# Kernel optimization log

Measured on AMD Instinct MI355X. Metric: run time of the kernel, lower is better.

Reference implementation:

```python
import jax, jax.numpy as jnp
import numpy as np

GROUP_SIZE = 128
ZERO_POINT = 8  # 4-bit symmetric zero point


def setup_inputs() -> dict:
    key = jax.random.key(0)
    k1, k2, k3, k4, k5, k6 = jax.random.split(key, 6)
    B, S, IN, OUT, RANK = 4, 2048, 4096, 4096, 32
    n_groups = IN // GROUP_SIZE  # 32
    x = jax.random.normal(k1, (B, S, IN), dtype=jnp.float32)
    q = jax.random.randint(k2, (OUT, IN), 0, 16, dtype=jnp.int32)  # 4-bit codes
    scales = jax.random.uniform(k3, (OUT, n_groups), dtype=jnp.float32)
    U = jax.random.normal(k4, (OUT, RANK), dtype=jnp.float32)
    V = jax.random.normal(k5, (RANK, IN), dtype=jnp.float32)
    bias = jax.random.normal(k6, (OUT,), dtype=jnp.float32)
    return {"x": x, "q": q, "scales": scales, "U": U, "V": V, "bias": bias}


def reference(x, q, scales, U, V, bias):
    out_f, in_f = q.shape
    n_groups = scales.shape[1]
    # Dequantize: per-group scaled 4-bit codes -> [out, in]
    qf = (q.astype(scales.dtype) - ZERO_POINT).reshape(out_f, n_groups, GROUP_SIZE)
    W = (qf * scales[:, :, None]).reshape(out_f, in_f)
    # Low-rank correction
    W = W + U @ V
    # F.linear: y = x @ W^T + b
    return jnp.einsum("bsi,oi->bso", x, W) + bias
```

## Files before the change

### kernel.cpp

```cpp
#include <hip/hip_runtime.h>
#include <hip/hip_bf16.h>

#define GAS __attribute__((address_space(1)))
#define LAS __attribute__((address_space(3)))

typedef __bf16 bf16x8 __attribute__((ext_vector_type(8)));
typedef float f32x4 __attribute__((ext_vector_type(4)));

constexpr int Kd = 4096;
constexpr int Nd = 4096;
constexpr int RANKd = 32;
constexpr int NGroups = 32;
constexpr int BM = 128, BN = 128, BK = 32;

constexpr int BWR = 32;
constexpr int BWC = 256;

__global__ __launch_bounds__(256) void build_w(
    const int* __restrict__ q, const float* __restrict__ scales,
    const float* __restrict__ U, const float* __restrict__ V,
    __hip_bfloat16* __restrict__ W)
{
  __shared__ float V_s[RANKd][BWC + 4];
  __shared__ float U_s[BWR][RANKd + 1];

  const int t  = threadIdx.x;
  const int n0 = blockIdx.y * BWR;
  const int k0 = blockIdx.x * BWC;

  {
    const int idx = t * 4;
    const int row = idx >> 5, rr = idx & 31;
    float4 uv = *(const float4*)(U + (size_t)(n0 + row) * RANKd + rr);
    U_s[row][rr] = uv.x; U_s[row][rr + 1] = uv.y;
    U_s[row][rr + 2] = uv.z; U_s[row][rr + 3] = uv.w;
  }
  #pragma unroll
  for (int i = 0; i < 8; ++i) {
    const int idx = i * 1024 + t * 4;
    const int vr = idx >> 8, vc = idx & 255;
    float4 vv = *(const float4*)(V + (size_t)vr * Kd + k0 + vc);
    *(float4*)&V_s[vr][vc] = vv;
  }
  __syncthreads();

  const int rs   = t >> 5;
  const int cs   = t & 31;
  const int row0 = n0 + rs * 4;
  const int kc   = k0 + cs * 8;
  const int grp  = kc >> 7;

  float acc[4][8];
  #pragma unroll
  for (int j = 0; j < 4; ++j) {
    const int4* q4 = (const int4*)(q + (size_t)(row0 + j) * Kd + kc);
    int4 a = q4[0], b = q4[1];
    const float sc = scales[(size_t)(row0 + j) * NGroups + grp];
    acc[j][0] = (float)(a.x - 8) * sc; acc[j][1] = (float)(a.y - 8) * sc;
    acc[j][2] = (float)(a.z - 8) * sc; acc[j][3] = (float)(a.w - 8) * sc;
    acc[j][4] = (float)(b.x - 8) * sc; acc[j][5] = (float)(b.y - 8) * sc;
    acc[j][6] = (float)(b.z - 8) * sc; acc[j][7] = (float)(b.w - 8) * sc;
  }

  #pragma unroll 4
  for (int r = 0; r < RANKd; ++r) {
    float4 v0 = *(const float4*)&V_s[r][cs * 8];
    float4 v1 = *(const float4*)&V_s[r][cs * 8 + 4];
    #pragma unroll
    for (int j = 0; j < 4; ++j) {
      const float u = U_s[rs * 4 + j][r];
      acc[j][0] += u * v0.x; acc[j][1] += u * v0.y;
      acc[j][2] += u * v0.z; acc[j][3] += u * v0.w;
      acc[j][4] += u * v1.x; acc[j][5] += u * v1.y;
      acc[j][6] += u * v1.z; acc[j][7] += u * v1.w;
    }
  }

  #pragma unroll
  for (int j = 0; j < 4; ++j) {
    union { __hip_bfloat16 h[8]; int4 v; } o;
    #pragma unroll
    for (int i = 0; i < 8; ++i) o.h[i] = __float2bfloat16(acc[j][i]);
    *(int4*)(W + (size_t)(row0 + j) * Kd + kc) = o.v;
  }
}

__global__ __launch_bounds__(256) void convert_x(
    const float* __restrict__ x, __hip_bfloat16* __restrict__ xb)
{
  const size_t i = ((size_t)blockIdx.x * 256 + threadIdx.x) * 8;
  float4 a = *(const float4*)(x + i);
  float4 b = *(const float4*)(x + i + 4);
  union { __hip_bfloat16 h[8]; int4 v; } u;
  u.h[0] = __float2bfloat16(a.x); u.h[1] = __float2bfloat16(a.y);
  u.h[2] = __float2bfloat16(a.z); u.h[3] = __float2bfloat16(a.w);
  u.h[4] = __float2bfloat16(b.x); u.h[5] = __float2bfloat16(b.y);
  u.h[6] = __float2bfloat16(b.z); u.h[7] = __float2bfloat16(b.w);
  *(int4*)(xb + i) = u.v;
}

template <bool ABF16>
__global__ __launch_bounds__(256) void gemm_bt(
    const void* __restrict__ Ap, const __hip_bfloat16* __restrict__ Bt,
    const float* __restrict__ bias, float* __restrict__ C)
{
  __shared__ __hip_bfloat16 As[BM * BK];
  __shared__ __hip_bfloat16 Bs[BN * BK];

  const int t  = threadIdx.x;
  const int l  = t & 63;
  const int w  = t >> 6;
  const int wm = w >> 1;
  const int wn = w & 1;
  const int bm0 = blockIdx.y * BM;
  const int bn0 = blockIdx.x * BN;

  f32x4 acc[4][4];
  #pragma unroll
  for (int i = 0; i < 4; ++i)
    #pragma unroll
    for (int j = 0; j < 4; ++j)
      acc[i][j] = (f32x4){0.f, 0.f, 0.f, 0.f};

  const __hip_bfloat16* Abf = (const __hip_bfloat16*)Ap;
  const float*          A32 = (const float*)Ap;

  const int srow  = w * 16 + (l >> 2);
  const int schnk = (l & 3) ^ ((l >> 3) & 3);
  const __hip_bfloat16* ag0 = Abf + (size_t)(bm0 + srow) * Kd + schnk * 8;
  const __hip_bfloat16* bg0 = Bt  + (size_t)(bn0 + srow) * Kd + schnk * 8;
  char* asb = (char*)As + w * 1024;
  char* bsb = (char*)Bs + w * 1024;

  const int arow = t >> 1;
  const int apair = (t & 1);
  const float* a32p = A32 + (size_t)(bm0 + arow) * Kd + apair * 16;
  const int aswz = (arow >> 1) & 3;
  __hip_bfloat16* asw0 = As + arow * BK + (((apair * 2 + 0) ^ aswz) * 8);
  __hip_bfloat16* asw1 = As + arow * BK + (((apair * 2 + 1) ^ aswz) * 8);

  const int rlow = l & 15;
  const int rd_a = (wm * 64 + rlow) * 64 + (((l >> 4) ^ ((l >> 1) & 3)) * 16);
  const int rd_b = (wn * 64 + rlow) * 64 + (((l >> 4) ^ ((l >> 1) & 3)) * 16);

  for (int kt = 0; kt < Kd / BK; ++kt) {
    if constexpr (ABF16) {
      const __hip_bfloat16* ag = ag0 + kt * BK;
      __builtin_amdgcn_global_load_lds((GAS void*)ag,           (LAS void*)asb,          16, 0, 0);
      __builtin_amdgcn_global_load_lds((GAS void*)(ag + 64*Kd), (LAS void*)(asb + 4096), 16, 0, 0);
    } else {
      const float* ap = a32p + kt * BK;
      float4 f0 = ((const float4*)ap)[0];
      float4 f1 = ((const float4*)ap)[1];
      union { __hip_bfloat16 h[8]; int4 v; } u0, u1;
      u0.h[0]=__float2bfloat16(f0.x); u0.h[1]=__float2bfloat16(f0.y);
      u0.h[2]=__float2bfloat16(f0.z); u0.h[3]=__float2bfloat16(f0.w);
      u1.h[0]=__float2bfloat16(f1.x); u1.h[1]=__float2bfloat16(f1.y);
      u1.h[2]=__float2bfloat16(f1.z); u1.h[3]=__float2bfloat16(f1.w);
      *(int4*)asw0 = u0.v;
      *(int4*)asw1 = u1.v;
    }
    {
      const __hip_bfloat16* bg = bg0 + kt * BK;
      __builtin_amdgcn_global_load_lds((GAS void*)bg,           (LAS void*)bsb,          16, 0, 0);
      __builtin_amdgcn_global_load_lds((GAS void*)(bg + 64*Kd), (LAS void*)(bsb + 4096), 16, 0, 0);
    }

    __syncthreads();

    bf16x8 af[4], bf[4];
    #pragma unroll
    for (int i = 0; i < 4; ++i)
      af[i] = *(const bf16x8*)((const char*)As + rd_a + i * 1024);
    #pragma unroll
    for (int j = 0; j < 4; ++j)
      bf[j] = *(const bf16x8*)((const char*)Bs + rd_b + j * 1024);

    #pragma unroll
    for (int i = 0; i < 4; ++i)
      #pragma unroll
      for (int j = 0; j < 4; ++j)
        acc[i][j] = __builtin_amdgcn_mfma_f32_16x16x32_bf16(af[i], bf[j], acc[i][j], 0, 0, 0);

    __syncthreads();
  }

  const int colbase = bn0 + wn * 64 + (l & 15);
  const int rowbase = bm0 + wm * 64 + (l >> 4) * 4;
  #pragma unroll
  for (int j = 0; j < 4; ++j) {
    const int col = colbase + j * 16;
    const float bz = bias[col];
    #pragma unroll
    for (int i = 0; i < 4; ++i) {
      const int row0 = rowbase + i * 16;
      #pragma unroll
      for (int r = 0; r < 4; ++r)
        C[(size_t)(row0 + r) * Nd + col] = acc[i][j][r] + bz;
    }
  }
}

extern "C" void kernel_launch(void* const* d_in, const int* in_sizes, int n_in,
                              void* d_out, int out_size, void* d_ws, size_t ws_size,
                              hipStream_t stream)
{
  const float* x      = (const float*)d_in[0];
  const int*   q      = (const int*)  d_in[1];
  const float* scales = (const float*)d_in[2];
  const float* U      = (const float*)d_in[3];
  const float* V      = (const float*)d_in[4];
  const float* bias   = (const float*)d_in[5];
  float* out = (float*)d_out;

  const int M = in_sizes[0] / Kd;

  __hip_bfloat16* Wb = (__hip_bfloat16*)d_ws;
  const size_t wbytes = (size_t)Nd * Kd * sizeof(__hip_bfloat16);
  const size_t xbytes = (size_t)M  * Kd * sizeof(__hip_bfloat16);

  build_w<<<dim3(Kd / BWC, Nd / BWR), dim3(256), 0, stream>>>(q, scales, U, V, Wb);

  dim3 grid(Nd / BN, M / BM);
  if (ws_size >= wbytes + xbytes) {
    __hip_bfloat16* Xb = (__hip_bfloat16*)((char*)d_ws + wbytes);
    const int nconv = (M * (Kd / 8)) / 256;
    convert_x<<<dim3(nconv), dim3(256), 0, stream>>>(x, Xb);
    gemm_bt<true><<<grid, dim3(256), 0, stream>>>((const void*)Xb, Wb, bias, out);
  } else {
    gemm_bt<false><<<grid, dim3(256), 0, stream>>>((const void*)x, Wb, bias, out);
  }
}
```

Measured before the change: 604.4 us.

## Switch GEMM to 32x32x16 MFMA with BK=64, fuse W build and x conversion

The GEMM now uses 32x32x16 bf16 MFMA with a 2x2 tile per wave and a K-tile of 64, plus a new XOR swizzle for the wider LDS rows. This issues fewer MFMAs and LDS reads per unit of work and halves the number of barrier-synchronised K iterations. The weight-build and x-conversion kernels are merged into one prep launch to save a launch and let both run at once. Build-w now writes 8-byte chunks split across two groups, and the larger LDS tile and 16-float accumulators may raise register and LDS pressure.

```diff
diff --git a/kernel.cpp b/kernel.cpp
--- a/kernel.cpp
+++ b/kernel.cpp
@@ -5,28 +5,50 @@
 #define LAS __attribute__((address_space(3)))
 
 typedef __bf16 bf16x8 __attribute__((ext_vector_type(8)));
-typedef float f32x4 __attribute__((ext_vector_type(4)));
+typedef float f32x16 __attribute__((ext_vector_type(16)));
 
 constexpr int Kd = 4096;
 constexpr int Nd = 4096;
 constexpr int RANKd = 32;
-constexpr int NGroups = 32;
-constexpr int BM = 128, BN = 128, BK = 32;
-
-constexpr int BWR = 32;
-constexpr int BWC = 256;
-
-__global__ __launch_bounds__(256) void build_w(
+constexpr int NG = 32;
+constexpr int BM = 128, BN = 128, BK = 64;
+
+constexpr int BWR = 32, BWC = 256;
+constexpr int NBUILD = (Nd / BWR) * (Kd / BWC);
+
+__global__ __launch_bounds__(256) void prep(
     const int* __restrict__ q, const float* __restrict__ scales,
     const float* __restrict__ U, const float* __restrict__ V,
-    __hip_bfloat16* __restrict__ W)
+    __hip_bfloat16* __restrict__ W,
+    const float* __restrict__ x, __hip_bfloat16* __restrict__ xb)
 {
   __shared__ float V_s[RANKd][BWC + 4];
   __shared__ float U_s[BWR][RANKd + 1];
 
-  const int t  = threadIdx.x;
-  const int n0 = blockIdx.y * BWR;
-  const int k0 = blockIdx.x * BWC;
+  const int t = threadIdx.x;
+  const int bid = blockIdx.x;
+
+  if (bid >= NBUILD) {
+    const size_t base = (size_t)(bid - NBUILD) * 8192;
+    #pragma unroll
+    for (int i = 0; i < 4; ++i) {
+      const size_t idx = base + i * 2048 + t * 8;
+      float4 a = *(const float4*)(x + idx);
+      float4 b = *(const float4*)(x + idx + 4);
+      union { __hip_bfloat16 h[8]; int4 v; } u;
+      u.h[0] = __float2bfloat16(a.x); u.h[1] = __float2bfloat16(a.y);
+      u.h[2] = __float2bfloat16(a.z); u.h[3] = __float2bfloat16(a.w);
+      u.h[4] = __float2bfloat16(b.x); u.h[5] = __float2bfloat16(b.y);
+      u.h[6] = __float2bfloat16(b.z); u.h[7] = __float2bfloat16(b.w);
+      *(int4*)(xb + idx) = u.v;
+    }
+    return;
+  }
+
+  const int bx = bid & 15;
+  const int by = bid >> 4;
+  const int n0 = by * BWR;
+  const int k0 = bx * BWC;
 
   {
     const int idx = t * 4;
@@ -39,33 +61,35 @@
   for (int i = 0; i < 8; ++i) {
     const int idx = i * 1024 + t * 4;
     const int vr = idx >> 8, vc = idx & 255;
-    float4 vv = *(const float4*)(V + (size_t)vr * Kd + k0 + vc);
-    *(float4*)&V_s[vr][vc] = vv;
+    *(float4*)&V_s[vr][vc] = *(const float4*)(V + (size_t)vr * Kd + k0 + vc);
   }
   __syncthreads();
 
-  const int rs   = t >> 5;
-  const int cs   = t & 31;
+  const int rs = t >> 5;
+  const int cs = t & 31;
   const int row0 = n0 + rs * 4;
-  const int kc   = k0 + cs * 8;
-  const int grp  = kc >> 7;
+  const int c0 = cs * 4;
+  const int c1 = 128 + cs * 4;
+  const int g0 = k0 >> 7, g1 = g0 + 1;
 
   float acc[4][8];
   #pragma unroll
   for (int j = 0; j < 4; ++j) {
-    const int4* q4 = (const int4*)(q + (size_t)(row0 + j) * Kd + kc);
-    int4 a = q4[0], b = q4[1];
-    const float sc = scales[(size_t)(row0 + j) * NGroups + grp];
-    acc[j][0] = (float)(a.x - 8) * sc; acc[j][1] = (float)(a.y - 8) * sc;
-    acc[j][2] = (float)(a.z - 8) * sc; acc[j][3] = (float)(a.w - 8) * sc;
-    acc[j][4] = (float)(b.x - 8) * sc; acc[j][5] = (float)(b.y - 8) * sc;
-    acc[j][6] = (float)(b.z - 8) * sc; acc[j][7] = (float)(b.w - 8) * sc;
+    const int* qr = q + (size_t)(row0 + j) * Kd + k0;
+    int4 a = *(const int4*)(qr + c0);
+    int4 b = *(const int4*)(qr + c1);
+    const float s0 = scales[(size_t)(row0 + j) * NG + g0];
+    const float s1 = scales[(size_t)(row0 + j) * NG + g1];
+    acc[j][0] = (float)(a.x - 8) * s0; acc[j][1] = (float)(a.y - 8) * s0;
+    acc[j][2] = (float)(a.z - 8) * s0; acc[j][3] = (float)(a.w - 8) * s0;
+    acc[j][4] = (float)(b.x - 8) * s1; acc[j][5] = (float)(b.y - 8) * s1;
+    acc[j][6] = (float)(b.z - 8) * s1; acc[j][7] = (float)(b.w - 8) * s1;
   }
 
   #pragma unroll 4
   for (int r = 0; r < RANKd; ++r) {
-    float4 v0 = *(const float4*)&V_s[r][cs * 8];
-    float4 v1 = *(const float4*)&V_s[r][cs * 8 + 4];
+    float4 v0 = *(const float4*)&V_s[r][c0];
+    float4 v1 = *(const float4*)&V_s[r][c1];
     #pragma unroll
     for (int j = 0; j < 4; ++j) {
       const float u = U_s[rs * 4 + j][r];
@@ -78,25 +102,15 @@
 
   #pragma unroll
   for (int j = 0; j < 4; ++j) {
-    union { __hip_bfloat16 h[8]; int4 v; } o;
-    #pragma unroll
-    for (int i = 0; i < 8; ++i) o.h[i] = __float2bfloat16(acc[j][i]);
-    *(int4*)(W + (size_t)(row0 + j) * Kd + kc) = o.v;
-  }
-}
-
-__global__ __launch_bounds__(256) void convert_x(
-    const float* __restrict__ x, __hip_bfloat16* __restrict__ xb)
-{
-  const size_t i = ((size_t)blockIdx.x * 256 + threadIdx.x) * 8;
-  float4 a = *(const float4*)(x + i);
-  float4 b = *(const float4*)(x + i + 4);
-  union { __hip_bfloat16 h[8]; int4 v; } u;
-  u.h[0] = __float2bfloat16(a.x); u.h[1] = __float2bfloat16(a.y);
-  u.h[2] = __float2bfloat16(a.z); u.h[3] = __float2bfloat16(a.w);
-  u.h[4] = __float2bfloat16(b.x); u.h[5] = __float2bfloat16(b.y);
-  u.h[6] = __float2bfloat16(b.z); u.h[7] = __float2bfloat16(b.w);
-  *(int4*)(xb + i) = u.v;
+    union { __hip_bfloat16 h[4]; uint2 v; } o0, o1;
+    o0.h[0] = __float2bfloat16(acc[j][0]); o0.h[1] = __float2bfloat16(acc[j][1]);
+    o0.h[2] = __float2bfloat16(acc[j][2]); o0.h[3] = __float2bfloat16(acc[j][3]);
+    o1.h[0] = __float2bfloat16(acc[j][4]); o1.h[1] = __float2bfloat16(acc[j][5]);
+    o1.h[2] = __float2bfloat16(acc[j][6]); o1.h[3] = __float2bfloat16(acc[j][7]);
+    __hip_bfloat16* wr = W + (size_t)(row0 + j) * Kd + k0;
+    *(uint2*)(wr + c0) = o0.v;
+    *(uint2*)(wr + c1) = o1.v;
+  }
 }
 
 template <bool ABF16>
@@ -115,88 +129,99 @@
   const int bm0 = blockIdx.y * BM;
   const int bn0 = blockIdx.x * BN;
 
-  f32x4 acc[4][4];
-  #pragma unroll
-  for (int i = 0; i < 4; ++i)
-    #pragma unroll
-    for (int j = 0; j < 4; ++j)
-      acc[i][j] = (f32x4){0.f, 0.f, 0.f, 0.f};
+  f32x16 acc[2][2];
+  #pragma unroll
+  for (int i = 0; i < 2; ++i)
+    #pragma unroll
+    for (int j = 0; j < 2; ++j)
+      acc[i][j] = (f32x16)(0.f);
 
   const __hip_bfloat16* Abf = (const __hip_bfloat16*)Ap;
   const float*          A32 = (const float*)Ap;
 
-  const int srow  = w * 16 + (l >> 2);
-  const int schnk = (l & 3) ^ ((l >> 3) & 3);
-  const __hip_bfloat16* ag0 = Abf + (size_t)(bm0 + srow) * Kd + schnk * 8;
-  const __hip_bfloat16* bg0 = Bt  + (size_t)(bn0 + srow) * Kd + schnk * 8;
-  char* asb = (char*)As + w * 1024;
-  char* bsb = (char*)Bs + w * 1024;
-
-  const int arow = t >> 1;
-  const int apair = (t & 1);
-  const float* a32p = A32 + (size_t)(bm0 + arow) * Kd + apair * 16;
-  const int aswz = (arow >> 1) & 3;
-  __hip_bfloat16* asw0 = As + arow * BK + (((apair * 2 + 0) ^ aswz) * 8);
-  __hip_bfloat16* asw1 = As + arow * BK + (((apair * 2 + 1) ^ aswz) * 8);
-
-  const int rlow = l & 15;
-  const int rd_a = (wm * 64 + rlow) * 64 + (((l >> 4) ^ ((l >> 1) & 3)) * 16);
-  const int rd_b = (wn * 64 + rlow) * 64 + (((l >> 4) ^ ((l >> 1) & 3)) * 16);
+  const int srow = l >> 3;
+  const int schk = (l & 7) ^ srow;
+  const __hip_bfloat16* ag0 = Abf + (size_t)(bm0 + w * 32 + srow) * Kd + schk * 8;
+  const __hip_bfloat16* bg0 = Bt  + (size_t)(bn0 + w * 32 + srow) * Kd + schk * 8;
+  char* asb = (char*)As + w * 32 * 128;
+  char* bsb = (char*)Bs + w * 32 * 128;
+
+  const int rl = l & 31, kh = l >> 5, rx = rl & 7;
+  const char* Ard = (const char*)As + (wm * 64 + rl) * 128;
+  const char* Brd = (const char*)Bs + (wn * 64 + rl) * 128;
+
+  const int arow = t >> 1, ahalf = t & 1, arx = arow & 7;
+  const float* a32p = A32 + (size_t)(bm0 + arow) * Kd + ahalf * 32;
+  char* awr = (char*)As + arow * 128;
 
   for (int kt = 0; kt < Kd / BK; ++kt) {
     if constexpr (ABF16) {
       const __hip_bfloat16* ag = ag0 + kt * BK;
-      __builtin_amdgcn_global_load_lds((GAS void*)ag,           (LAS void*)asb,          16, 0, 0);
-      __builtin_amdgcn_global_load_lds((GAS void*)(ag + 64*Kd), (LAS void*)(asb + 4096), 16, 0, 0);
+      #pragma unroll
+      for (int s = 0; s < 4; ++s)
+        __builtin_amdgcn_global_load_lds((GAS void*)(ag + s * 8 * Kd),
+                                         (LAS void*)(asb + s * 1024), 16, 0, 0);
     } else {
       const float* ap = a32p + kt * BK;
-      float4 f0 = ((const float4*)ap)[0];
-      float4 f1 = ((const float4*)ap)[1];
-      union { __hip_bfloat16 h[8]; int4 v; } u0, u1;
-      u0.h[0]=__float2bfloat16(f0.x); u0.h[1]=__float2bfloat16(f0.y);
-      u0.h[2]=__float2bfloat16(f0.z); u0.h[3]=__float2bfloat16(f0.w);
-      u1.h[0]=__float2bfloat16(f1.x); u1.h[1]=__float2bfloat16(f1.y);
-      u1.h[2]=__float2bfloat16(f1.z); u1.h[3]=__float2bfloat16(f1.w);
-      *(int4*)asw0 = u0.v;
-      *(int4*)asw1 = u1.v;
+      #pragma unroll
+      for (int cc = 0; cc < 4; ++cc) {
+        float4 f0 = ((const float4*)ap)[cc * 2];
+        float4 f1 = ((const float4*)ap)[cc * 2 + 1];
+        union { __hip_bfloat16 h[8]; int4 v; } u;
+        u.h[0] = __float2bfloat16(f0.x); u.h[1] = __float2bfloat16(f0.y);
+        u.h[2] = __float2bfloat16(f0.z); u.h[3] = __float2bfloat16(f0.w);
+        u.h[4] = __float2bfloat16(f1.x); u.h[5] = __float2bfloat16(f1.y);
+        u.h[6] = __float2bfloat16(f1.z); u.h[7] = __float2bfloat16(f1.w);
+        const int c = ahalf * 4 + cc;
+        *(int4*)(awr + ((c ^ arx) * 16)) = u.v;
+      }
     }
     {
       const __hip_bfloat16* bg = bg0 + kt * BK;
-      __builtin_amdgcn_global_load_lds((GAS void*)bg,           (LAS void*)bsb,          16, 0, 0);
-      __builtin_amdgcn_global_load_lds((GAS void*)(bg + 64*Kd), (LAS void*)(bsb + 4096), 16, 0, 0);
+      #pragma unroll
+      for (int s = 0; s < 4; ++s)
+        __builtin_amdgcn_global_load_lds((GAS void*)(bg + s * 8 * Kd),
+                                         (LAS void*)(bsb + s * 1024), 16, 0, 0);
     }
 
     __syncthreads();
 
-    bf16x8 af[4], bf[4];
-    #pragma unroll
-    for (int i = 0; i < 4; ++i)
-      af[i] = *(const bf16x8*)((const char*)As + rd_a + i * 1024);
-    #pragma unroll
-    for (int j = 0; j < 4; ++j)
-      bf[j] = *(const bf16x8*)((const char*)Bs + rd_b + j * 1024);
-
-    #pragma unroll
-    for (int i = 0; i < 4; ++i)
-      #pragma unroll
-      for (int j = 0; j < 4; ++j)
-        acc[i][j] = __builtin_amdgcn_mfma_f32_16x16x32_bf16(af[i], bf[j], acc[i][j], 0, 0, 0);
+    bf16x8 af[2][4], bfr[2][4];
+    #pragma unroll
+    for (int mi = 0; mi < 2; ++mi)
+      #pragma unroll
+      for (int ks = 0; ks < 4; ++ks)
+        af[mi][ks] = *(const bf16x8*)(Ard + mi * 4096 + (((ks * 2 + kh) ^ rx) * 16));
+    #pragma unroll
+    for (int nj = 0; nj < 2; ++nj)
+      #pragma unroll
+      for (int ks = 0; ks < 4; ++ks)
+        bfr[nj][ks] = *(const bf16x8*)(Brd + nj * 4096 + (((ks * 2 + kh) ^ rx) * 16));
+
+    #pragma unroll
+    for (int ks = 0; ks < 4; ++ks)
+      #pragma unroll
+      for (int mi = 0; mi < 2; ++mi)
+        #pragma unroll
+        for (int nj = 0; nj < 2; ++nj)
+          acc[mi][nj] = __builtin_amdgcn_mfma_f32_32x32x16_bf16(
+              af[mi][ks], bfr[nj][ks], acc[mi][nj], 0, 0, 0);
 
     __syncthreads();
   }
 
-  const int colbase = bn0 + wn * 64 + (l & 15);
-  const int rowbase = bm0 + wm * 64 + (l >> 4) * 4;
-  #pragma unroll
-  for (int j = 0; j < 4; ++j) {
-    const int col = colbase + j * 16;
+  #pragma unroll
+  for (int nj = 0; nj < 2; ++nj) {
+    const int col = bn0 + wn * 64 + nj * 32 + rl;
     const float bz = bias[col];
     #pragma unroll
-    for (int i = 0; i < 4; ++i) {
-      const int row0 = rowbase + i * 16;
-      #pragma unroll
-      for (int r = 0; r < 4; ++r)
-        C[(size_t)(row0 + r) * Nd + col] = acc[i][j][r] + bz;
+    for (int mi = 0; mi < 2; ++mi) {
+      const int rbase = bm0 + wm * 64 + mi * 32 + 4 * kh;
+      #pragma unroll
+      for (int reg = 0; reg < 16; ++reg) {
+        const int row = rbase + (reg & 3) + 8 * (reg >> 2);
+        C[(size_t)row * Nd + col] = acc[mi][nj][reg] + bz;
+      }
     }
   }
 }
@@ -219,15 +244,14 @@
   const size_t wbytes = (size_t)Nd * Kd * sizeof(__hip_bfloat16);
   const size_t xbytes = (size_t)M  * Kd * sizeof(__hip_bfloat16);
 
-  build_w<<<dim3(Kd / BWC, Nd / BWR), dim3(256), 0, stream>>>(q, scales, U, V, Wb);
-
   dim3 grid(Nd / BN, M / BM);
   if (ws_size >= wbytes + xbytes) {
     __hip_bfloat16* Xb = (__hip_bfloat16*)((char*)d_ws + wbytes);
-    const int nconv = (M * (Kd / 8)) / 256;
-    convert_x<<<dim3(nconv), dim3(256), 0, stream>>>(x, Xb);
+    const int nconv = (int)(((size_t)M * Kd) / 8192);
+    prep<<<dim3(NBUILD + nconv), dim3(256), 0, stream>>>(q, scales, U, V, Wb, x, Xb);
     gemm_bt<true><<<grid, dim3(256), 0, stream>>>((const void*)Xb, Wb, bias, out);
   } else {
+    prep<<<dim3(NBUILD), dim3(256), 0, stream>>>(q, scales, U, V, Wb, x, nullptr);
     gemm_bt<false><<<grid, dim3(256), 0, stream>>>((const void*)x, Wb, bias, out);
   }
 }
```

Result: faster. 581.3 us (-3.8%).
